# Optimization experiments

Measured on AMD Instinct MI355X. Metric: run time of the kernel, lower is better.

Reference implementation:

```python
import jax, jax.numpy as jnp
import numpy as np

B = 16384
D_IN = 1024
D_OUT = 512
H1 = 4 * D_IN      # floor(layersDimentions[0]*inputDimention) = 4096
H3 = 4 * D_OUT     # floor(layersDimentions[1]*outputDimention) = 2048
H4 = 4 * D_OUT     # floor(layersDimentions[2]*outputDimention) = 2048
M = 256            # codebook size


def _linear_params(key, fan_in, fan_out):
    kw, kb = jax.random.split(key)
    bound = 1.0 / np.sqrt(fan_in)
    w = jax.random.uniform(kw, (fan_out, fan_in), jnp.float32, -bound, bound)
    b = jax.random.uniform(kb, (fan_out,), jnp.float32, -bound, bound)
    return w, b


def setup_inputs() -> dict:
    key = jax.random.key(0)
    ks = jax.random.split(key, 7)
    x = jax.random.normal(ks[0], (B, D_IN), jnp.float32)
    codebook = jnp.sort(jax.random.normal(ks[1], (M,), jnp.float32))
    w1, b1 = _linear_params(ks[2], D_IN, H1)
    w2, b2 = _linear_params(ks[3], H1, D_OUT)
    w3, b3 = _linear_params(ks[4], D_OUT, H3)
    w4, b4 = _linear_params(ks[5], H3, H4)
    w5, b5 = _linear_params(ks[6], H4, D_OUT)
    return {"x": x, "codebook": codebook,
            "w1": w1, "b1": b1, "w2": w2, "b2": b2,
            "w3": w3, "b3": b3, "w4": w4, "b4": b4,
            "w5": w5, "b5": b5}


def _quantize(x, codebook):
    # nearest codeword per scalar element: argmin_m |x - c_m|
    # x: [B, D], codebook: [M]
    d = jnp.abs(x[..., None] - codebook)          # [B, D, M]
    idx = jnp.argmin(d, axis=-1)                  # [B, D]
    return codebook[idx]


def reference(x, codebook, w1, b1, w2, b2, w3, b3, w4, b4, w5, b5):
    h = x @ w1.T + b1                # [B, H1]
    h = h @ w2.T + b2                # [B, D_OUT]
    h = _quantize(h, codebook)       # [B, D_OUT]
    h = h @ w3.T + b3                # [B, H3]
    h = h @ w4.T + b4                # [B, H4]
    return h @ w5.T + b5             # [B, D_OUT]
```

## Files before the change

kernel.cpp:

```cpp
#include <hip/hip_runtime.h>


typedef __bf16 v8bf __attribute__((ext_vector_type(8)));
typedef float  v4f  __attribute__((ext_vector_type(4)));

#define Bdim   16384
#define DIN    1024
#define DOUT   512
#define H1dim  4096
#define H3dim  2048
#define H4dim  2048

#define GLOBAL_AS __attribute__((address_space(1)))
#define LDS_AS    __attribute__((address_space(3)))

__device__ __forceinline__ void load16_to_lds(const __bf16* g, __bf16* l) {
  __builtin_amdgcn_global_load_lds((const GLOBAL_AS unsigned int*)g,
                                   (LDS_AS unsigned int*)l, 16, 0, 0);
}

__device__ __forceinline__ unsigned pack2bf(float a, float b) {
  return (unsigned)__builtin_bit_cast(unsigned short, (__bf16)a) |
         ((unsigned)__builtin_bit_cast(unsigned short, (__bf16)b) << 16);
}

__device__ __forceinline__ void transpose_body(const float* __restrict__ in,
                                               __bf16* __restrict__ out,
                                               int R, int C, int bx, int by,
                                               float (*tile)[68]) {
  const int c0 = bx * 32, r0 = by * 64;
  const int t = threadIdx.x, tr = t >> 5, tc = t & 31;
#pragma unroll
  for (int i = 0; i < 8; ++i)
    tile[tc][tr + i * 8] = in[(size_t)(r0 + tr + i * 8) * C + (c0 + tc)];
  __syncthreads();
  const int orow = t >> 3, oc = (t & 7) * 8;
  float4 a = *(const float4*)&tile[orow][oc];
  float4 b = *(const float4*)&tile[orow][oc + 4];
  int4 o;
  o.x = pack2bf(a.x, a.y); o.y = pack2bf(a.z, a.w);
  o.z = pack2bf(b.x, b.y); o.w = pack2bf(b.z, b.w);
  *(int4*)&out[(size_t)(c0 + orow) * R + (r0 + oc)] = o;
}

__device__ __forceinline__ void cast16_body(const float* __restrict__ in,
                                            __bf16* __restrict__ out, int b) {
  const size_t i = (size_t)b * 4096 + (size_t)threadIdx.x * 16;
  float4 a0 = *(const float4*)&in[i];
  float4 a1 = *(const float4*)&in[i + 4];
  float4 a2 = *(const float4*)&in[i + 8];
  float4 a3 = *(const float4*)&in[i + 12];
  int4 o0, o1;
  o0.x = pack2bf(a0.x, a0.y); o0.y = pack2bf(a0.z, a0.w);
  o0.z = pack2bf(a1.x, a1.y); o0.w = pack2bf(a1.z, a1.w);
  o1.x = pack2bf(a2.x, a2.y); o1.y = pack2bf(a2.z, a2.w);
  o1.z = pack2bf(a3.x, a3.y); o1.w = pack2bf(a3.z, a3.w);
  *(int4*)&out[i] = o0;
  *(int4*)&out[i + 8] = o1;
}

__global__ void prepw_kernel(const float* __restrict__ w1, __bf16* __restrict__ w1T,
                             const float* __restrict__ w4, __bf16* __restrict__ w4T,
                             const float* __restrict__ w3, __bf16* __restrict__ w3T,
                             const float* __restrict__ w2, __bf16* __restrict__ w2b,
                             const float* __restrict__ w5, __bf16* __restrict__ w5b) {
  __shared__ float tile[32][68];
  int b = blockIdx.x;
  if (b < 2048) {
    transpose_body(w1, w1T, H1dim, DIN, b & 31, b >> 5, tile);
  } else if (b < 4096) {
    b -= 2048;
    transpose_body(w4, w4T, H4dim, H3dim, b & 63, b >> 6, tile);
  } else if (b < 4608) {
    b -= 4096;
    transpose_body(w3, w3T, H3dim, DOUT, b & 15, b >> 4, tile);
  } else if (b < 5120) {
    cast16_body(w2, w2b, b - 4608);
  } else {
    cast16_body(w5, w5b, b - 5120);
  }
}

__device__ __forceinline__ void bias_ba_body(int bb, const float* __restrict__ b1,
                                             const float* __restrict__ w2,
                                             const float* __restrict__ b2,
                                             float* __restrict__ ba) {
  const int wave = threadIdx.x >> 6, lane = threadIdx.x & 63;
  const int j = bb * 4 + wave;
  float s = 0.f;
  for (int k = lane; k < H1dim; k += 64) s += b1[k] * w2[(size_t)j * H1dim + k];
#pragma unroll
  for (int off = 32; off; off >>= 1) s += __shfl_xor(s, off, 64);
  if (lane == 0) ba[j] = s + b2[j];
}

__device__ __forceinline__ void bias_bc_body(int bb, const float* __restrict__ b3,
                                             const __bf16* __restrict__ WtT,
                                             const float* __restrict__ b4,
                                             const float* __restrict__ w5,
                                             const float* __restrict__ b5,
                                             float* __restrict__ bc) {
  const int wave = threadIdx.x >> 6, lane = threadIdx.x & 63;
  const int j = bb * 4 + wave;
  float s = 0.f;
  for (int k = lane; k < H4dim; k += 64)
    s += b3[k] * (float)WtT[(size_t)j * H4dim + k] + b4[k] * w5[(size_t)j * H4dim + k];
#pragma unroll
  for (int off = 32; off; off >>= 1) s += __shfl_xor(s, off, 64);
  if (lane == 0) bc[j] = s + b5[j];
}

enum { MODE_W = 0, MODE_Q = 1, MODE_OUT = 2 };

#define ASM_BAR() asm volatile("s_barrier" ::: "memory")

template <int MODE, int BM>
__device__ __forceinline__ void gemm_body(__bf16* As, __bf16* Bs, float* cbs,
                                          int bx, int by,
                                          const __bf16* __restrict__ A,
                                          const __bf16* __restrict__ Bt,
                                          void* __restrict__ Cout,
                                          const float* __restrict__ bias,
                                          const float* __restrict__ codebook,
                                          int M, int N, int K, int CH) {
  const int t = threadIdx.x;
  const int m0 = bx * BM, n0 = by * 64;
  if constexpr (MODE == MODE_Q) cbs[t] = codebook[t];

  const int lane = t & 63, wave = t >> 6;
  const int quad = lane >> 4, l15 = lane & 15;
  constexpr int MI = BM / 32;
  const int wm = (wave & 1) * (BM / 2), wn = (wave >> 1) * 32;

  const int lrow = lane >> 3;
  const int gcol = ((lane & 7) ^ lrow) * 8;
  const __bf16* gA = A  + (size_t)(m0 + (BM / 4) * wave + lrow) * K + gcol;
  const __bf16* gB = Bt + (size_t)(n0 + 16 * wave + lrow) * K + gcol;
  const int swz = l15 & 7;

  v4f acc[MI][2], accT[MI][2];
#pragma unroll
  for (int i = 0; i < MI; ++i)
#pragma unroll
    for (int j = 0; j < 2; ++j) {
      acc[i][j] = (v4f){0.f, 0.f, 0.f, 0.f};
      if constexpr (MODE == MODE_W) accT[i][j] = (v4f){0.f, 0.f, 0.f, 0.f};
    }

  auto stage = [&](int k0, int buf) {
    __bf16* lA = As + buf * (BM * 64) + (BM / 4) * wave * 64;
    __bf16* lB = Bs + buf * (64 * 64) + 16 * wave * 64;
#pragma unroll
    for (int p = 0; p < MI; ++p)
      load16_to_lds(gA + (size_t)(8 * p) * K + k0, lA + p * 512);
#pragma unroll
    for (int p = 0; p < 2; ++p)
      load16_to_lds(gB + (size_t)(8 * p) * K + k0, lB + p * 512);
  };

  const int nk = K >> 6;
  const int chsteps = CH >> 6;
  stage(0, 0);
  stage(64, 1);

  int cc = 0;
  for (int tk = 0; tk < nk; ++tk) {
    if (tk + 1 < nk) {
      if constexpr (BM == 128) asm volatile("s_waitcnt vmcnt(6)" ::: "memory");
      else                     asm volatile("s_waitcnt vmcnt(4)" ::: "memory");
    } else {
      asm volatile("s_waitcnt vmcnt(0)" ::: "memory");
    }
    ASM_BAR();

    const __bf16* cA = As + (tk & 1) * (BM * 64);
    const __bf16* cB = Bs + (tk & 1) * (64 * 64);
#pragma unroll
    for (int kk = 0; kk < 2; ++kk) {
      const int cch = ((kk * 4 + quad) ^ swz) * 8;
      v8bf af[MI], bv[2];
#pragma unroll
      for (int i = 0; i < MI; ++i)
        af[i] = *(const v8bf*)&cA[(wm + i * 16 + l15) * 64 + cch];
#pragma unroll
      for (int j = 0; j < 2; ++j)
        bv[j] = *(const v8bf*)&cB[(wn + j * 16 + l15) * 64 + cch];
#pragma unroll
      for (int i = 0; i < MI; ++i)
#pragma unroll
        for (int j = 0; j < 2; ++j)
          acc[i][j] = __builtin_amdgcn_mfma_f32_16x16x32_bf16(af[i], bv[j], acc[i][j], 0, 0, 0);
    }
    if constexpr (MODE == MODE_W) {
      if (++cc == chsteps) {
        cc = 0;
#pragma unroll
        for (int i = 0; i < MI; ++i)
#pragma unroll
          for (int j = 0; j < 2; ++j) {
            accT[i][j] += acc[i][j];
            acc[i][j] = (v4f){0.f, 0.f, 0.f, 0.f};
          }
      }
    }
    asm volatile("s_waitcnt lgkmcnt(0)" ::: "memory");
    ASM_BAR();
    if (tk + 2 < nk) stage((tk + 2) << 6, tk & 1);
  }

#pragma unroll
  for (int j = 0; j < 2; ++j) {
    const int gn = n0 + wn + j * 16 + l15;
    float bj = 0.f;
    if constexpr (MODE != MODE_W) bj = bias[gn];
#pragma unroll
    for (int i = 0; i < MI; ++i) {
#pragma unroll
      for (int r = 0; r < 4; ++r) {
        const int gm = m0 + wm + i * 16 + quad * 4 + r;
        if constexpr (MODE == MODE_W) {
          ((__bf16*)Cout)[(size_t)gm * N + gn] = (__bf16)accT[i][j][r];
        } else if constexpr (MODE == MODE_Q) {
          float v = acc[i][j][r] + bj;
          int idx = 0;
#pragma unroll
          for (int s = 128; s > 0; s >>= 1) {
            const int u = idx + s;
            if (cbs[u] <= v) idx = u;
          }
          float best = cbs[idx];
          if (idx < 255) {
            const float c1 = cbs[idx + 1];
            if (!(v - best <= c1 - v)) best = c1;
          }
          ((__bf16*)Cout)[(size_t)gm * N + gn] = (__bf16)best;
        } else {
          ((float*)Cout)[(size_t)gm * N + gn] = acc[i][j][r] + bj;
        }
      }
    }
  }
}

__global__ __launch_bounds__(256, 3)
void foldA_kernel(const __bf16* __restrict__ w2b, const __bf16* __restrict__ w1T,
                  __bf16* __restrict__ WaT,
                  const __bf16* __restrict__ w5b, const __bf16* __restrict__ w4T,
                  __bf16* __restrict__ WtT,
                  const float* __restrict__ b1, const float* __restrict__ w2,
                  const float* __restrict__ b2, float* __restrict__ ba,
                  const float* __restrict__ x, __bf16* __restrict__ xb) {
  __shared__ __align__(16) __bf16 As[2 * 64 * 64];
  __shared__ __align__(16) __bf16 Bs[2 * 64 * 64];
  int b = blockIdx.x;
  if (b < 128) {
    const int c = b & 7, i = b >> 3;
    gemm_body<MODE_W, 64>(As, Bs, nullptr, i >> 1, c * 2 + (i & 1), w2b, w1T, WaT,
                          nullptr, nullptr, DOUT, DIN, H1dim, 512);
  } else if (b < 384) {
    b -= 128;
    const int c = b & 7, i = b >> 3;
    gemm_body<MODE_W, 64>(As, Bs, nullptr, i >> 2, c * 4 + (i & 3), w5b, w4T, WtT,
                          nullptr, nullptr, DOUT, H3dim, H4dim, 512);
  } else if (b < 512) {
    bias_ba_body(b - 384, b1, w2, b2, ba);
  } else {
    cast16_body(x, xb, b - 512);
  }
}

__global__ __launch_bounds__(256, 3)
void foldB_kernel(const __bf16* __restrict__ WtT, const __bf16* __restrict__ w3T,
                  __bf16* __restrict__ WcT,
                  const float* __restrict__ b3, const float* __restrict__ b4,
                  const float* __restrict__ w5, const float* __restrict__ b5,
                  float* __restrict__ bc,
                  const __bf16* __restrict__ xb, const __bf16* __restrict__ WaT,
                  __bf16* __restrict__ q, const float* __restrict__ ba,
                  const float* __restrict__ cb) {
  __shared__ __align__(16) __bf16 As[2 * 128 * 64];
  __shared__ __align__(16) __bf16 Bs[2 * 64 * 64];
  __shared__ float cbs[256];
  int b = blockIdx.x;
  if (b < 64) {
    const int c = b & 7, i = b >> 3;
    gemm_body<MODE_W, 64>(As, Bs, nullptr, i, c, WtT, w3T, WcT,
                          nullptr, nullptr, DOUT, DOUT, H3dim, 256);
  } else if (b < 192) {
    bias_bc_body(b - 64, b3, WtT, b4, w5, b5, bc);
  } else {
    b -= 192;
    const int c = b & 7, i = b >> 3;
    gemm_body<MODE_Q, 128>(As, Bs, cbs, c * 16 + (i >> 3), i & 7, xb, WaT, q,
                           ba, cb, Bdim, DOUT, DIN, DIN);
  }
}

__global__ __launch_bounds__(256, 3)
void gemmout_kernel(const __bf16* __restrict__ q, const __bf16* __restrict__ WcT,
                    float* __restrict__ out, const float* __restrict__ bc) {
  __shared__ __align__(16) __bf16 As[2 * 128 * 64];
  __shared__ __align__(16) __bf16 Bs[2 * 64 * 64];
  const int b = blockIdx.x;
  const int c = b & 7, i = b >> 3;
  gemm_body<MODE_OUT, 128>(As, Bs, nullptr, c * 16 + (i >> 3), i & 7,
                           q, WcT, out, bc, nullptr, Bdim, DOUT, DOUT, DOUT);
}

extern "C" void kernel_launch(void* const* d_in, const int* in_sizes, int n_in,
                              void* d_out, int out_size, void* d_ws, size_t ws_size,
                              hipStream_t stream) {
  const float* x  = (const float*)d_in[0];
  const float* cb = (const float*)d_in[1];
  const float* w1 = (const float*)d_in[2];
  const float* b1 = (const float*)d_in[3];
  const float* w2 = (const float*)d_in[4];
  const float* b2 = (const float*)d_in[5];
  const float* w3 = (const float*)d_in[6];
  const float* b3 = (const float*)d_in[7];
  const float* w4 = (const float*)d_in[8];
  const float* b4 = (const float*)d_in[9];
  const float* w5 = (const float*)d_in[10];
  const float* b5 = (const float*)d_in[11];
  float* out = (float*)d_out;

  char* ws = (char*)d_ws;
  size_t off = 0;
  auto alloc = [&](size_t bytes) -> void* {
    void* p = ws + off;
    off = (off + bytes + 255) & ~(size_t)255;
    return p;
  };
  __bf16* w1T = (__bf16*)alloc((size_t)DIN * H1dim * 2);
  __bf16* w4T = (__bf16*)alloc((size_t)H3dim * H4dim * 2);
  __bf16* w3T = (__bf16*)alloc((size_t)DOUT * H3dim * 2);
  __bf16* w2b = (__bf16*)alloc((size_t)DOUT * H1dim * 2);
  __bf16* w5b = (__bf16*)alloc((size_t)DOUT * H4dim * 2);
  __bf16* WaT = (__bf16*)alloc((size_t)DOUT * DIN * 2);
  __bf16* WtT = (__bf16*)alloc((size_t)DOUT * H3dim * 2);
  __bf16* WcT = (__bf16*)alloc((size_t)DOUT * DOUT * 2);
  __bf16* q   = (__bf16*)alloc((size_t)Bdim * DOUT * 2);
  __bf16* xb  = (__bf16*)alloc((size_t)Bdim * DIN * 2);
  float*  ba  = (float*)alloc(DOUT * 4);
  float*  bc  = (float*)alloc(DOUT * 4);

  prepw_kernel<<<5376, 256, 0, stream>>>(w1, w1T, w4, w4T, w3, w3T,
                                         w2, w2b, w5, w5b);

  foldA_kernel<<<4608, 256, 0, stream>>>(w2b, w1T, WaT, w5b, w4T, WtT,
                                         b1, w2, b2, ba, x, xb);

  foldB_kernel<<<1216, 256, 0, stream>>>(WtT, w3T, WcT, b3, b4, w5, b5, bc,
                                         xb, WaT, q, ba, cb);

  gemmout_kernel<<<1024, 256, 0, stream>>>(q, WcT, out, bc);
}
```

Baseline: 259.9 us.

## Split-K the weight-folding GEMMs into fp32 partials with a separate reduction kernel

The two weight-fold GEMMs (w2·w1 and w5·w4) used only 384 blocks, each running the full K dimension. They are now split along K into 8 and 4 slices, giving 2048 blocks that write fp32 partial products into scratch space borrowed from the output and q buffers. A new reduce kernel sums the partials and converts them to bf16. This trades an extra kernel launch and extra partial-sum memory traffic for much higher occupancy in the fold stage.

Measured after the change: 267.9 us. 3.1% more time.

```diff
diff --git a/kernel.cpp b/kernel.cpp
--- a/kernel.cpp
+++ b/kernel.cpp
@@ -110,7 +110,7 @@
   if (lane == 0) bc[j] = s + b5[j];
 }
 
-enum { MODE_W = 0, MODE_Q = 1, MODE_OUT = 2 };
+enum { MODE_W = 0, MODE_Q = 1, MODE_OUT = 2, MODE_P = 3 };
 
 #define ASM_BAR() asm volatile("s_barrier" ::: "memory")
 
@@ -122,7 +122,8 @@
                                           void* __restrict__ Cout,
                                           const float* __restrict__ bias,
                                           const float* __restrict__ codebook,
-                                          int M, int N, int K, int CH) {
+                                          int M, int N, int Kstride,
+                                          int Klen, int kbeg, int CH) {
   const int t = threadIdx.x;
   const int m0 = bx * BM, n0 = by * 64;
   if constexpr (MODE == MODE_Q) cbs[t] = codebook[t];
@@ -134,8 +135,8 @@
 
   const int lrow = lane >> 3;
   const int gcol = ((lane & 7) ^ lrow) * 8;
-  const __bf16* gA = A  + (size_t)(m0 + (BM / 4) * wave + lrow) * K + gcol;
-  const __bf16* gB = Bt + (size_t)(n0 + 16 * wave + lrow) * K + gcol;
+  const __bf16* gA = A  + (size_t)(m0 + (BM / 4) * wave + lrow) * Kstride + gcol;
+  const __bf16* gB = Bt + (size_t)(n0 + 16 * wave + lrow) * Kstride + gcol;
   const int swz = l15 & 7;
 
   v4f acc[MI][2], accT[MI][2];
@@ -144,7 +145,8 @@
 #pragma unroll
     for (int j = 0; j < 2; ++j) {
       acc[i][j] = (v4f){0.f, 0.f, 0.f, 0.f};
-      if constexpr (MODE == MODE_W) accT[i][j] = (v4f){0.f, 0.f, 0.f, 0.f};
+      if constexpr (MODE == MODE_W || MODE == MODE_P)
+        accT[i][j] = (v4f){0.f, 0.f, 0.f, 0.f};
     }
 
   auto stage = [&](int k0, int buf) {
@@ -152,16 +154,16 @@
     __bf16* lB = Bs + buf * (64 * 64) + 16 * wave * 64;
 #pragma unroll
     for (int p = 0; p < MI; ++p)
-      load16_to_lds(gA + (size_t)(8 * p) * K + k0, lA + p * 512);
+      load16_to_lds(gA + (size_t)(8 * p) * Kstride + k0, lA + p * 512);
 #pragma unroll
     for (int p = 0; p < 2; ++p)
-      load16_to_lds(gB + (size_t)(8 * p) * K + k0, lB + p * 512);
+      load16_to_lds(gB + (size_t)(8 * p) * Kstride + k0, lB + p * 512);
   };
 
-  const int nk = K >> 6;
+  const int nk = Klen >> 6;
   const int chsteps = CH >> 6;
-  stage(0, 0);
-  stage(64, 1);
+  stage(kbeg, 0);
+  stage(kbeg + 64, 1);
 
   int cc = 0;
   for (int tk = 0; tk < nk; ++tk) {
@@ -191,7 +193,7 @@
         for (int j = 0; j < 2; ++j)
           acc[i][j] = __builtin_amdgcn_mfma_f32_16x16x32_bf16(af[i], bv[j], acc[i][j], 0, 0, 0);
     }
-    if constexpr (MODE == MODE_W) {
+    if constexpr (MODE == MODE_W || MODE == MODE_P) {
       if (++cc == chsteps) {
         cc = 0;
 #pragma unroll
@@ -205,14 +207,14 @@
     }
     asm volatile("s_waitcnt lgkmcnt(0)" ::: "memory");
     ASM_BAR();
-    if (tk + 2 < nk) stage((tk + 2) << 6, tk & 1);
+    if (tk + 2 < nk) stage(kbeg + ((tk + 2) << 6), tk & 1);
   }
 
 #pragma unroll
   for (int j = 0; j < 2; ++j) {
     const int gn = n0 + wn + j * 16 + l15;
     float bj = 0.f;
-    if constexpr (MODE != MODE_W) bj = bias[gn];
+    if constexpr (MODE == MODE_Q || MODE == MODE_OUT) bj = bias[gn];
 #pragma unroll
     for (int i = 0; i < MI; ++i) {
 #pragma unroll
@@ -220,6 +222,8 @@
         const int gm = m0 + wm + i * 16 + quad * 4 + r;
         if constexpr (MODE == MODE_W) {
           ((__bf16*)Cout)[(size_t)gm * N + gn] = (__bf16)accT[i][j][r];
+        } else if constexpr (MODE == MODE_P) {
+          ((float*)Cout)[(size_t)gm * N + gn] = accT[i][j][r];
         } else if constexpr (MODE == MODE_Q) {
           float v = acc[i][j][r] + bj;
           int idx = 0;
@@ -244,29 +248,55 @@
 
 __global__ __launch_bounds__(256, 3)
 void foldA_kernel(const __bf16* __restrict__ w2b, const __bf16* __restrict__ w1T,
-                  __bf16* __restrict__ WaT,
+                  float* __restrict__ p1,
                   const __bf16* __restrict__ w5b, const __bf16* __restrict__ w4T,
-                  __bf16* __restrict__ WtT,
+                  float* __restrict__ p2,
                   const float* __restrict__ b1, const float* __restrict__ w2,
                   const float* __restrict__ b2, float* __restrict__ ba,
                   const float* __restrict__ x, __bf16* __restrict__ xb) {
   __shared__ __align__(16) __bf16 As[2 * 64 * 64];
   __shared__ __align__(16) __bf16 Bs[2 * 64 * 64];
   int b = blockIdx.x;
-  if (b < 128) {
-    const int c = b & 7, i = b >> 3;
-    gemm_body<MODE_W, 64>(As, Bs, nullptr, i >> 1, c * 2 + (i & 1), w2b, w1T, WaT,
-                          nullptr, nullptr, DOUT, DIN, H1dim, 512);
-  } else if (b < 384) {
-    b -= 128;
-    const int c = b & 7, i = b >> 3;
-    gemm_body<MODE_W, 64>(As, Bs, nullptr, i >> 2, c * 4 + (i & 3), w5b, w4T, WtT,
-                          nullptr, nullptr, DOUT, H3dim, H4dim, 512);
-  } else if (b < 512) {
-    bias_ba_body(b - 384, b1, w2, b2, ba);
+  if (b < 1024) {
+    const int z = b >> 7, b0 = b & 127;
+    const int c = b0 & 7, i = b0 >> 3;
+    gemm_body<MODE_P, 64>(As, Bs, nullptr, i >> 1, c * 2 + (i & 1), w2b, w1T,
+                          p1 + (size_t)z * DOUT * DIN, nullptr, nullptr,
+                          DOUT, DIN, H1dim, 512, z * 512, 512);
+  } else if (b < 2048) {
+    b -= 1024;
+    const int z = b >> 8, b1i = b & 255;
+    const int c = b1i & 7, i = b1i >> 3;
+    gemm_body<MODE_P, 64>(As, Bs, nullptr, i >> 2, c * 4 + (i & 3), w5b, w4T,
+                          p2 + (size_t)z * DOUT * H3dim, nullptr, nullptr,
+                          DOUT, H3dim, H4dim, 512, z * 512, 512);
+  } else if (b < 2176) {
+    bias_ba_body(b - 2048, b1, w2, b2, ba);
   } else {
-    cast16_body(x, xb, b - 512);
-  }
+    cast16_body(x, xb, b - 2176);
+  }
+}
+
+__device__ __forceinline__ void reduce_body(const float* __restrict__ part,
+                                            __bf16* __restrict__ out, int MN4, int S, int i) {
+  if (i >= MN4) return;
+  const float4* p = reinterpret_cast<const float4*>(part);
+  float4 s = p[i];
+  for (int k = 1; k < S; ++k) {
+    float4 v = p[(size_t)k * MN4 + i];
+    s.x += v.x; s.y += v.y; s.z += v.z; s.w += v.w;
+  }
+  uint2 o;
+  o.x = pack2bf(s.x, s.y);
+  o.y = pack2bf(s.z, s.w);
+  reinterpret_cast<uint2*>(out)[i] = o;
+}
+
+__global__ void foldR_kernel(const float* __restrict__ p1, __bf16* __restrict__ WaT,
+                             const float* __restrict__ p2, __bf16* __restrict__ WtT) {
+  const int b = blockIdx.x, t = threadIdx.x;
+  if (b < 512) reduce_body(p1, WaT, DOUT * DIN / 4, 8, b * 256 + t);
+  else         reduce_body(p2, WtT, DOUT * H3dim / 4, 4, (b - 512) * 256 + t);
 }
 
 __global__ __launch_bounds__(256, 3)
@@ -285,14 +315,14 @@
   if (b < 64) {
     const int c = b & 7, i = b >> 3;
     gemm_body<MODE_W, 64>(As, Bs, nullptr, i, c, WtT, w3T, WcT,
-                          nullptr, nullptr, DOUT, DOUT, H3dim, 256);
+                          nullptr, nullptr, DOUT, DOUT, H3dim, H3dim, 0, 256);
   } else if (b < 192) {
     bias_bc_body(b - 64, b3, WtT, b4, w5, b5, bc);
   } else {
     b -= 192;
     const int c = b & 7, i = b >> 3;
     gemm_body<MODE_Q, 128>(As, Bs, cbs, c * 16 + (i >> 3), i & 7, xb, WaT, q,
-                           ba, cb, Bdim, DOUT, DIN, DIN);
+                           ba, cb, Bdim, DOUT, DIN, DIN, 0, DIN);
   }
 }
 
@@ -304,7 +334,7 @@
   const int b = blockIdx.x;
   const int c = b & 7, i = b >> 3;
   gemm_body<MODE_OUT, 128>(As, Bs, nullptr, c * 16 + (i >> 3), i & 7,
-                           q, WcT, out, bc, nullptr, Bdim, DOUT, DOUT, DOUT);
+                           q, WcT, out, bc, nullptr, Bdim, DOUT, DOUT, DOUT, 0, DOUT);
 }
 
 extern "C" void kernel_launch(void* const* d_in, const int* in_sizes, int n_in,
@@ -343,12 +373,16 @@
   __bf16* xb  = (__bf16*)alloc((size_t)Bdim * DIN * 2);
   float*  ba  = (float*)alloc(DOUT * 4);
   float*  bc  = (float*)alloc(DOUT * 4);
+  float* p1 = (float*)d_out;
+  float* p2 = (float*)q;
 
   prepw_kernel<<<5376, 256, 0, stream>>>(w1, w1T, w4, w4T, w3, w3T,
                                          w2, w2b, w5, w5b);
 
-  foldA_kernel<<<4608, 256, 0, stream>>>(w2b, w1T, WaT, w5b, w4T, WtT,
+  foldA_kernel<<<6272, 256, 0, stream>>>(w2b, w1T, p1, w5b, w4T, p2,
                                          b1, w2, b2, ba, x, xb);
+
+  foldR_kernel<<<1536, 256, 0, stream>>>(p1, WaT, p2, WtT);
 
   foldB_kernel<<<1216, 256, 0, stream>>>(WtT, w3T, WcT, b3, b4, w5, b5, bc,
                                          xb, WaT, q, ba, cb);
```
